# Kernel optimization log

Hardware: AMD Instinct MI355X
Metric: run time of the kernel (lower is better)

The kernel has to match this reference:

```python
import jax, jax.numpy as jnp
import numpy as np

B, N, C = 8, 1024, 1024
H = 16
D = C // H  # head_dim = 64
SCALE = D ** -0.5


def setup_inputs() -> dict:
    key = jax.random.key(0)
    k1, k2, k3 = jax.random.split(key, 3)
    x = jax.random.normal(k1, (B, N, C), dtype=jnp.float32)
    w_qkv = jax.random.normal(k2, (3 * C, C), dtype=jnp.float32) * (C ** -0.5)
    w_proj = jax.random.normal(k3, (C, C), dtype=jnp.float32) * (C ** -0.5)
    b_proj = jnp.zeros((C,), dtype=jnp.float32)
    return {"x": x, "w_qkv": w_qkv, "w_proj": w_proj, "b_proj": b_proj}


def reference(x, w_qkv, w_proj, b_proj):
    Bx, Nx, Cx = x.shape
    # qkv: [B,N,3C] -> [3,B,H,N,D]
    qkv = jnp.einsum('bnc,oc->bno', x, w_qkv)
    qkv = qkv.reshape(Bx, Nx, 3, H, D).transpose(2, 0, 3, 1, 4)
    q, k, v = qkv[0], qkv[1], qkv[2]
    attn = jnp.einsum('bhnd,bhmd->bhnm', q, k) * SCALE  # [B,H,N,N]
    attn = jax.nn.softmax(attn, axis=-1)
    out = jnp.einsum('bhnm,bhmd->bhnd', attn, v)  # [B,H,N,D]
    out = out.transpose(0, 2, 1, 3).reshape(Bx, Nx, Cx)
    return jnp.einsum('bnc,oc->bno', out, w_proj) + b_proj
```

## Files before the change

kernel.cpp:

```cpp
#include <hip/hip_runtime.h>

typedef _Float16 half8 __attribute__((ext_vector_type(8)));
typedef _Float16 half4v __attribute__((ext_vector_type(4)));
typedef _Float16 half2v __attribute__((ext_vector_type(2)));
typedef float floatx4 __attribute__((ext_vector_type(4)));

#define AS3 __attribute__((address_space(3)))
#define AS1 __attribute__((address_space(1)))

static __device__ inline half2v pkrtz(float a, float b) {
    return __builtin_bit_cast(half2v, __builtin_amdgcn_cvt_pkrtz(a, b));
}

__global__ __launch_bounds__(256) void cvt_all(const float* __restrict__ x,
                                               const float* __restrict__ wq,
                                               const float* __restrict__ wp,
                                               _Float16* __restrict__ xh,
                                               _Float16* __restrict__ wqh,
                                               _Float16* __restrict__ wph) {
    long i = (long)blockIdx.x * 256 + threadIdx.x;
    const float4* src; half4v* dst; long off;
    if (i < 2097152)      { src = (const float4*)x;  dst = (half4v*)xh;  off = i; }
    else if (i < 2883584) { src = (const float4*)wq; dst = (half4v*)wqh; off = i - 2097152; }
    else                  { src = (const float4*)wp; dst = (half4v*)wph; off = i - 2883584; }
    float4 v = src[off];
    half4v h = {(_Float16)v.x, (_Float16)v.y, (_Float16)v.z, (_Float16)v.w};
    dst[off] = h;
}

__global__ __launch_bounds__(256, 3) void gemm_tn(
    const _Float16* __restrict__ A, const _Float16* __restrict__ B,
    _Float16* __restrict__ Ch, int ldc, _Float16* __restrict__ Vt, int split,
    float* __restrict__ Cf, const float* __restrict__ bias,
    int M, int Nn, int K)
{
    __shared__ _Float16 sA[2][128 * 32];
    __shared__ _Float16 sB[2][128 * 32];
    const int tid  = threadIdx.x;
    const int lane = tid & 63, wave = tid >> 6;
    const int quad = lane >> 4, l16 = lane & 15;
    const int wr = wave >> 1, wc = wave & 1;
    const long m0 = (long)blockIdx.x * 128, n0 = (long)blockIdx.y * 128;

    const int srow = tid >> 2;
    const int sslot = ((tid & 3) ^ ((srow >> 1) & 3)) * 8;
    const int dlo = srow * 32 + sslot;
    const int dhi = (srow + 64) * 32 + sslot;
    const _Float16* gA0 = A + (m0 + srow) * (long)K + (tid & 3) * 8;
    const _Float16* gA1 = A + (m0 + srow + 64) * (long)K + (tid & 3) * 8;
    const _Float16* gB0 = B + (n0 + srow) * (long)K + (tid & 3) * 8;
    const _Float16* gB1 = B + (n0 + srow + 64) * (long)K + (tid & 3) * 8;

    const int swz = (l16 >> 1) & 3;
    const int aoff = ((quad ^ swz) * 8);

    floatx4 acc[4][4] = {};
    const int nk = K >> 5;

    {
        half8 a0 = *(const half8*)gA0, a1 = *(const half8*)gA1;
        half8 b0 = *(const half8*)gB0, b1 = *(const half8*)gB1;
        *(half8*)&sA[0][dlo] = a0; *(half8*)&sA[0][dhi] = a1;
        *(half8*)&sB[0][dlo] = b0; *(half8*)&sB[0][dhi] = b1;
    }
    half8 pA0[2], pA1[2], pB0[2], pB1[2];
    pA0[0] = *(const half8*)(gA0 + 32); pA1[0] = *(const half8*)(gA1 + 32);
    pB0[0] = *(const half8*)(gB0 + 32); pB1[0] = *(const half8*)(gB1 + 32);

    for (int kk = 0; kk < nk; kk += 2) {
#pragma unroll
        for (int u = 0; u < 2; u++) {
            const int k = kk + u;
            __syncthreads();
            if (k + 2 < nk) {
                const long ko = (long)(k + 2) << 5;
                pA0[u ^ 1] = *(const half8*)(gA0 + ko);
                pA1[u ^ 1] = *(const half8*)(gA1 + ko);
                pB0[u ^ 1] = *(const half8*)(gB0 + ko);
                pB1[u ^ 1] = *(const half8*)(gB1 + ko);
            }

            const _Float16* cA = &sA[u][0];
            const _Float16* cB = &sB[u][0];
            half8 af[4], bf[4];
#pragma unroll
            for (int t = 0; t < 4; t++)
                af[t] = *(const half8*)&cA[(wr * 64 + t * 16 + l16) * 32 + aoff];
#pragma unroll
            for (int t = 0; t < 4; t++)
                bf[t] = *(const half8*)&cB[(wc * 64 + t * 16 + l16) * 32 + aoff];
#pragma unroll
            for (int tm = 0; tm < 4; tm++)
#pragma unroll
                for (int tn = 0; tn < 4; tn++)
                    acc[tm][tn] = __builtin_amdgcn_mfma_f32_16x16x32_f16(af[tm], bf[tn], acc[tm][tn], 0, 0, 0);

            if (k + 1 < nk) {
                _Float16* nA = &sA[u ^ 1][0];
                _Float16* nB = &sB[u ^ 1][0];
                *(half8*)&nA[dlo] = pA0[u];
                *(half8*)&nA[dhi] = pA1[u];
                *(half8*)&nB[dlo] = pB0[u];
                *(half8*)&nB[dhi] = pB1[u];
            }
        }
    }

#pragma unroll
    for (int tm = 0; tm < 4; tm++) {
        long row = m0 + wr * 64 + tm * 16 + quad * 4;
#pragma unroll
        for (int tn = 0; tn < 4; tn++) {
            long col = n0 + wc * 64 + tn * 16 + l16;
            if (Cf) {
                float bv = bias ? bias[col] : 0.f;
#pragma unroll
                for (int r = 0; r < 4; r++)
                    Cf[(row + r) * (long)Nn + col] = acc[tm][tn][r] + bv;
            } else if (col >= split) {
                long cv = col - split;
                long vrow = ((row >> 10) * 16 + (cv >> 6)) * 64 + (cv & 63);
                long nn = row & 1023;
                half4v pv = {(_Float16)acc[tm][tn][0], (_Float16)acc[tm][tn][1],
                             (_Float16)acc[tm][tn][2], (_Float16)acc[tm][tn][3]};
                *(half4v*)&Vt[vrow * 1024 + nn] = pv;
            } else {
#pragma unroll
                for (int r = 0; r < 4; r++)
                    Ch[(row + r) * (long)ldc + col] = (_Float16)acc[tm][tn][r];
            }
        }
    }
}

#define QSC 0.18033688f
__global__ __launch_bounds__(256, 4) void flash_attn(const _Float16* __restrict__ qk,
                                                     const _Float16* __restrict__ vt,
                                                     _Float16* __restrict__ out)
{
    const int bh = blockIdx.x, b = bh >> 4, h = bh & 15;
    const int n0 = blockIdx.y * 128;
    const int tid = threadIdx.x, lane = tid & 63, wave = tid >> 6;
    const int quad = lane >> 4, l16 = lane & 15;

    __shared__ _Float16 sK[64 * 72];
    __shared__ _Float16 sVT[64 * 72];
    __shared__ _Float16 sPT[4][32 * 72];

    half8 qf[2][2];
    const _Float16 qs = (_Float16)QSC;
    const _Float16* qbase = qk + (long)(b * 1024 + n0 + wave * 32) * 2048 + h * 64;
#pragma unroll
    for (int t = 0; t < 2; t++)
#pragma unroll
        for (int s = 0; s < 2; s++) {
            half8 v = *(const half8*)(qbase + (long)(t * 16 + l16) * 2048 + s * 32 + quad * 8);
#pragma unroll
            for (int j = 0; j < 8; j++) v[j] *= qs;
            qf[t][s] = v;
        }

    const int srow = tid >> 3, scol8 = (tid & 7) * 8;
    const _Float16* kgb = qk + 1024 + h * 64 + scol8 + (long)(b * 1024 + srow) * 2048;
    const _Float16* vgb = vt + (long)(bh * 64 + srow) * 1024 + scol8;

    float l_[2] = {0.f, 0.f};
    floatx4 o[2][4] = {};
    const floatx4 fzero = {0.f, 0.f, 0.f, 0.f};

    for (int kt = 0; kt < 16; kt++) {
        const int kr0 = kt * 64;
        __syncthreads();
#pragma unroll
        for (int i = 0; i < 2; i++) {
            int r = srow + i * 32;
            *(half8*)&sK[r * 72 + scol8]  = *(const half8*)(kgb + (long)(kr0 + i * 32) * 2048);
            *(half8*)&sVT[r * 72 + scol8] = *(const half8*)(vgb + (long)(i * 32) * 1024 + kr0);
        }
        __syncthreads();

#pragma unroll
        for (int c = 0; c < 4; c++) {
            half8 kf0 = *(const half8*)&sK[(c * 16 + l16) * 72 + quad * 8];
            half8 kf1 = *(const half8*)&sK[(c * 16 + l16) * 72 + 32 + quad * 8];
#pragma unroll
            for (int t = 0; t < 2; t++) {
                floatx4 a = __builtin_amdgcn_mfma_f32_16x16x32_f16(kf0, qf[t][0], fzero, 0, 0, 0);
                a = __builtin_amdgcn_mfma_f32_16x16x32_f16(kf1, qf[t][1], a, 0, 0, 0);
                float p0 = exp2f(a[0]), p1 = exp2f(a[1]);
                float p2 = exp2f(a[2]), p3 = exp2f(a[3]);
                l_[t] += (p0 + p1) + (p2 + p3);
                half2v lo = pkrtz(p0, p1);
                half2v hi = pkrtz(p2, p3);
                half4v pk = __builtin_shufflevector(lo, hi, 0, 1, 2, 3);
                *(half4v*)&sPT[wave][(t * 16 + l16) * 72 + c * 16 + quad * 4] = pk;
            }
        }

#pragma unroll
        for (int kk = 0; kk < 2; kk++) {
            half8 pf0 = *(const half8*)&sPT[wave][(l16) * 72 + kk * 32 + quad * 8];
            half8 pf1 = *(const half8*)&sPT[wave][(16 + l16) * 72 + kk * 32 + quad * 8];
#pragma unroll
            for (int dt = 0; dt < 4; dt++) {
                half8 vf = *(const half8*)&sVT[(dt * 16 + l16) * 72 + kk * 32 + quad * 8];
                o[0][dt] = __builtin_amdgcn_mfma_f32_16x16x32_f16(vf, pf0, o[0][dt], 0, 0, 0);
                o[1][dt] = __builtin_amdgcn_mfma_f32_16x16x32_f16(vf, pf1, o[1][dt], 0, 0, 0);
            }
        }
    }

#pragma unroll
    for (int t = 0; t < 2; t++) {
        float rs = l_[t];
        rs += __shfl_xor(rs, 16);
        rs += __shfl_xor(rs, 32);
        float inv = 1.f / rs;
#pragma unroll
        for (int dt = 0; dt < 4; dt++) {
            floatx4 v = o[t][dt];
            half2v lo = pkrtz(v[0] * inv, v[1] * inv);
            half2v hi = pkrtz(v[2] * inv, v[3] * inv);
            half4v a = __builtin_shufflevector(lo, hi, 0, 1, 2, 3);
            *(half4v*)&sPT[wave][(t * 16 + l16) * 72 + dt * 16 + quad * 4] = a;
        }
    }
    __syncthreads();
#pragma unroll
    for (int i = 0; i < 4; i++) {
        int ql = i * 8 + (lane >> 3);
        int c8 = (lane & 7) * 8;
        half8 vv = *(const half8*)&sPT[wave][ql * 72 + c8];
        *(half8*)(out + (long)(b * 1024 + n0 + wave * 32 + ql) * 1024 + h * 64 + c8) = vv;
    }
}

extern "C" void kernel_launch(void* const* d_in, const int* in_sizes, int n_in,
                              void* d_out, int out_size, void* d_ws, size_t ws_size,
                              hipStream_t stream) {
    const float* x      = (const float*)d_in[0];
    const float* w_qkv  = (const float*)d_in[1];
    const float* w_proj = (const float*)d_in[2];
    const float* b_proj = (const float*)d_in[3];

    char* ws = (char*)d_ws;
    _Float16* qkh    = (_Float16*)ws;
    _Float16* vT     = (_Float16*)(ws + 33554432);
    _Float16* xh     = (_Float16*)(ws + 50331648);
    _Float16* wqkvh  = (_Float16*)(ws + 67108864);
    _Float16* wprojh = (_Float16*)(ws + 73400320);
    _Float16* attnh  = xh;

    cvt_all<<<12288, 256, 0, stream>>>(x, w_qkv, w_proj, xh, wqkvh, wprojh);

    gemm_tn<<<dim3(64, 24), 256, 0, stream>>>(xh, wqkvh, qkh, 2048, vT, 2048,
                                              nullptr, nullptr, 8192, 3072, 1024);
    flash_attn<<<dim3(128, 8), 256, 0, stream>>>(qkh, vT, attnh);
    gemm_tn<<<dim3(64, 8), 256, 0, stream>>>(attnh, wprojh, nullptr, 0, nullptr, 1 << 30,
                                             (float*)d_out, b_proj, 8192, 1024, 1024);
}
```

Measured before the change: 254.5 us.

## Prefetch K/V tiles in registers and add smaller-tile projection GEMM

The attention kernel now loads the next K and V^T tiles into registers right after the barrier, so global loads overlap the current tile's MFMA and softmax work instead of stalling before the shared-memory store. The output projection gets its own 64x128-tile kernel with occupancy hint 4, which launches 1024 blocks instead of 512 to fill the CUs better. The generic GEMM sheds its float-output branch. The costs are extra registers for the prefetch and more B-tile reloads in the projection.

Measured after the change: 254.8 us. No clear change (+0.1%).

```diff
diff --git a/kernel.cpp b/kernel.cpp
--- a/kernel.cpp
+++ b/kernel.cpp
@@ -31,7 +31,6 @@
 __global__ __launch_bounds__(256, 3) void gemm_tn(
     const _Float16* __restrict__ A, const _Float16* __restrict__ B,
     _Float16* __restrict__ Ch, int ldc, _Float16* __restrict__ Vt, int split,
-    float* __restrict__ Cf, const float* __restrict__ bias,
     int M, int Nn, int K)
 {
     __shared__ _Float16 sA[2][128 * 32];
@@ -112,12 +111,7 @@
 #pragma unroll
         for (int tn = 0; tn < 4; tn++) {
             long col = n0 + wc * 64 + tn * 16 + l16;
-            if (Cf) {
-                float bv = bias ? bias[col] : 0.f;
-#pragma unroll
-                for (int r = 0; r < 4; r++)
-                    Cf[(row + r) * (long)Nn + col] = acc[tm][tn][r] + bv;
-            } else if (col >= split) {
+            if (col >= split) {
                 long cv = col - split;
                 long vrow = ((row >> 10) * 16 + (cv >> 6)) * 64 + (cv & 63);
                 long nn = row & 1023;
@@ -129,6 +123,94 @@
                 for (int r = 0; r < 4; r++)
                     Ch[(row + r) * (long)ldc + col] = (_Float16)acc[tm][tn][r];
             }
+        }
+    }
+}
+
+__global__ __launch_bounds__(256, 4) void gemm_proj(
+    const _Float16* __restrict__ A, const _Float16* __restrict__ B,
+    float* __restrict__ Cf, const float* __restrict__ bias,
+    int Nn, int K)
+{
+    __shared__ _Float16 sA[2][64 * 32];
+    __shared__ _Float16 sB[2][128 * 32];
+    const int tid  = threadIdx.x;
+    const int lane = tid & 63, wave = tid >> 6;
+    const int quad = lane >> 4, l16 = lane & 15;
+    const int wr = wave >> 1, wc = wave & 1;
+    const long m0 = (long)blockIdx.x * 64, n0 = (long)blockIdx.y * 128;
+
+    const int srow = tid >> 2;
+    const int sslot = ((tid & 3) ^ ((srow >> 1) & 3)) * 8;
+    const int dlo = srow * 32 + sslot;
+    const int dhi = (srow + 64) * 32 + sslot;
+    const _Float16* gA0 = A + (m0 + srow) * (long)K + (tid & 3) * 8;
+    const _Float16* gB0 = B + (n0 + srow) * (long)K + (tid & 3) * 8;
+    const _Float16* gB1 = B + (n0 + srow + 64) * (long)K + (tid & 3) * 8;
+
+    const int swz = (l16 >> 1) & 3;
+    const int aoff = ((quad ^ swz) * 8);
+
+    floatx4 acc[2][4] = {};
+    const int nk = K >> 5;
+
+    {
+        half8 a0 = *(const half8*)gA0;
+        half8 b0 = *(const half8*)gB0, b1 = *(const half8*)gB1;
+        *(half8*)&sA[0][dlo] = a0;
+        *(half8*)&sB[0][dlo] = b0; *(half8*)&sB[0][dhi] = b1;
+    }
+    half8 pA0[2], pB0[2], pB1[2];
+    pA0[0] = *(const half8*)(gA0 + 32);
+    pB0[0] = *(const half8*)(gB0 + 32); pB1[0] = *(const half8*)(gB1 + 32);
+
+    for (int kk = 0; kk < nk; kk += 2) {
+#pragma unroll
+        for (int u = 0; u < 2; u++) {
+            const int k = kk + u;
+            __syncthreads();
+            if (k + 2 < nk) {
+                const long ko = (long)(k + 2) << 5;
+                pA0[u ^ 1] = *(const half8*)(gA0 + ko);
+                pB0[u ^ 1] = *(const half8*)(gB0 + ko);
+                pB1[u ^ 1] = *(const half8*)(gB1 + ko);
+            }
+
+            const _Float16* cA = &sA[u][0];
+            const _Float16* cB = &sB[u][0];
+            half8 af[2], bf[4];
+#pragma unroll
+            for (int t = 0; t < 2; t++)
+                af[t] = *(const half8*)&cA[(wr * 32 + t * 16 + l16) * 32 + aoff];
+#pragma unroll
+            for (int t = 0; t < 4; t++)
+                bf[t] = *(const half8*)&cB[(wc * 64 + t * 16 + l16) * 32 + aoff];
+#pragma unroll
+            for (int tm = 0; tm < 2; tm++)
+#pragma unroll
+                for (int tn = 0; tn < 4; tn++)
+                    acc[tm][tn] = __builtin_amdgcn_mfma_f32_16x16x32_f16(af[tm], bf[tn], acc[tm][tn], 0, 0, 0);
+
+            if (k + 1 < nk) {
+                _Float16* nA = &sA[u ^ 1][0];
+                _Float16* nB = &sB[u ^ 1][0];
+                *(half8*)&nA[dlo] = pA0[u];
+                *(half8*)&nB[dlo] = pB0[u];
+                *(half8*)&nB[dhi] = pB1[u];
+            }
+        }
+    }
+
+#pragma unroll
+    for (int tm = 0; tm < 2; tm++) {
+        long row = m0 + wr * 32 + tm * 16 + quad * 4;
+#pragma unroll
+        for (int tn = 0; tn < 4; tn++) {
+            long col = n0 + wc * 64 + tn * 16 + l16;
+            float bv = bias[col];
+#pragma unroll
+            for (int r = 0; r < 4; r++)
+                Cf[(row + r) * (long)Nn + col] = acc[tm][tn][r] + bv;
         }
     }
 }
@@ -168,16 +250,29 @@
     floatx4 o[2][4] = {};
     const floatx4 fzero = {0.f, 0.f, 0.f, 0.f};
 
+    half8 kreg[2], vreg[2];
+#pragma unroll
+    for (int i = 0; i < 2; i++) {
+        kreg[i] = *(const half8*)(kgb + (long)(i * 32) * 2048);
+        vreg[i] = *(const half8*)(vgb + (long)(i * 32) * 1024);
+    }
+
     for (int kt = 0; kt < 16; kt++) {
-        const int kr0 = kt * 64;
         __syncthreads();
 #pragma unroll
         for (int i = 0; i < 2; i++) {
-            int r = srow + i * 32;
-            *(half8*)&sK[r * 72 + scol8]  = *(const half8*)(kgb + (long)(kr0 + i * 32) * 2048);
-            *(half8*)&sVT[r * 72 + scol8] = *(const half8*)(vgb + (long)(i * 32) * 1024 + kr0);
+            *(half8*)&sK[(srow + i * 32) * 72 + scol8]  = kreg[i];
+            *(half8*)&sVT[(srow + i * 32) * 72 + scol8] = vreg[i];
         }
         __syncthreads();
+        if (kt + 1 < 16) {
+            const int kr1 = (kt + 1) * 64;
+#pragma unroll
+            for (int i = 0; i < 2; i++) {
+                kreg[i] = *(const half8*)(kgb + (long)(kr1 + i * 32) * 2048);
+                vreg[i] = *(const half8*)(vgb + (long)(i * 32) * 1024 + kr1);
+            }
+        }
 
 #pragma unroll
         for (int c = 0; c < 4; c++) {
@@ -254,8 +349,8 @@
     cvt_all<<<12288, 256, 0, stream>>>(x, w_qkv, w_proj, xh, wqkvh, wprojh);
 
     gemm_tn<<<dim3(64, 24), 256, 0, stream>>>(xh, wqkvh, qkh, 2048, vT, 2048,
-                                              nullptr, nullptr, 8192, 3072, 1024);
+                                              8192, 3072, 1024);
     flash_attn<<<dim3(128, 8), 256, 0, stream>>>(qkh, vT, attnh);
-    gemm_tn<<<dim3(64, 8), 256, 0, stream>>>(attnh, wprojh, nullptr, 0, nullptr, 1 << 30,
-                                             (float*)d_out, b_proj, 8192, 1024, 1024);
-}
+    gemm_proj<<<dim3(128, 8), 256, 0, stream>>>(attnh, wprojh, (float*)d_out, b_proj,
+                                                1024, 1024);
+}
```
